# Kernel tuning notes

Measured on AMD Instinct MI355X. Metric: run time of the kernel, lower is better.

## Reference

```python
import jax, jax.numpy as jnp
import numpy as np

NT = 256
T = 8192

def setup_inputs() -> dict:
    key = jax.random.key(0)
    k1, k2, k3, k4, k5 = jax.random.split(key, 5)
    emit = jax.random.normal(k1, (T, NT), dtype=jnp.float32)
    y = jax.random.randint(k2, (T,), 0, NT, dtype=jnp.int64)
    trans = jax.random.normal(k3, (NT, NT), dtype=jnp.float32)
    BOS = jax.random.normal(k4, (NT,), dtype=jnp.float32)
    EOS = jax.random.normal(k5, (NT,), dtype=jnp.float32)
    return {"emit": emit, "y": y, "trans": trans, "BOS": BOS, "EOS": EOS}

def _log_z(emit, trans, BOS):
    # alpha recurrence: alpha_new[j] = emit_i[j] + logsumexp_k(trans[k, j] + alpha[k])
    alpha0 = BOS + emit[0]
    def step(alpha, emit_i):
        alpha_new = emit_i + jax.nn.logsumexp(trans + alpha[:, None], axis=0)
        return alpha_new, None
    alpha, _ = jax.lax.scan(step, alpha0, emit[1:])
    return jax.nn.logsumexp(alpha)

def _gold_score(emit, y, trans, BOS, EOS):
    T_ = emit.shape[0]
    idx = jnp.arange(T_ - 1)
    s = BOS[y[0]]
    # faithful to original: emit[i, y[i]] for i in 0..T-2, plus trans[y[i], y[i+1]]
    s = s + jnp.sum(trans[y[:-1], y[1:]]) + jnp.sum(emit[idx, y[:-1]])
    s = s + EOS[y[-1]] + emit[-1, y[-1]]
    return s

def reference(emit, y, trans, BOS, EOS):
    logZ = _log_z(emit, trans, BOS)
    return logZ - _gold_score(emit, y, trans, BOS, EOS)
```

## Files before the change

kernel.cpp:

```cpp
#include <hip/hip_runtime.h>
#include <hip/hip_fp16.h>

#define TLEN 8192
#define NTS  256
#define CLEN 32
#define NCH  256
#define SLOT2 66048

typedef __bf16 bf16x8 __attribute__((ext_vector_type(8)));
typedef float  f32x4  __attribute__((ext_vector_type(4)));
union U128 { uint4 u; bf16x8 v; };
union U64  { uint2 u; long l; };

__device__ __forceinline__ unsigned f2bfu(float x) {
    unsigned u = __float_as_uint(x);
    return (u + 0x7fffu + ((u >> 16) & 1u)) >> 16;
}
__device__ __forceinline__ unsigned pk2(float lo, float hi) {
    return f2bfu(lo) | (f2bfu(hi) << 16);
}
__device__ __forceinline__ float bf2f(unsigned short h) {
    return __uint_as_float(((unsigned)h) << 16);
}
__device__ __forceinline__ unsigned pk4bf8(float a, float b, float c, float d) {
    int r = __builtin_amdgcn_cvt_pk_bf8_f32(a, b, 0, false);
    r = __builtin_amdgcn_cvt_pk_bf8_f32(c, d, r, true);
    return (unsigned)r;
}

__global__ __launch_bounds__(256, 2) void crf_phase1(
        const float* __restrict__ emit, const float* __restrict__ trans,
        char* __restrict__ outX) {
    __shared__ alignas(16) char qt8[65536];
    __shared__ alignas(16) char scr[4][1280];
    __shared__ alignas(16) float eld[2][NTS];

    const int t    = threadIdx.x;
    const int lane = t & 63;
    const int w    = t >> 6;
    const int gl   = lane >> 4;
    const int ln15 = lane & 15;
    const int c    = blockIdx.x >> 1;
    const int h    = blockIdx.x & 1;
    const int istart = (c == 0) ? 1 : CLEN * c;
    const int iend   = CLEN * c + CLEN;

    {
        const int ln = t & 15;
        for (int gk = 0; gk < 32; gk++) {
            float v[8];
            #pragma unroll
            for (int e = 0; e < 8; e++) v[e] = __expf(trans[(gk * 8 + e) * NTS + t]);
            uint2 u;
            u.x = pk4bf8(v[0], v[1], v[2], v[3]);
            u.y = pk4bf8(v[4], v[5], v[6], v[7]);
            const int p = (gk + 4 * ln + (ln >> 2)) & 31;
            *(uint2*)(qt8 + t * 256 + p * 8) = u;
        }
    }
    eld[istart & 1][t] = __expf(emit[istart * NTS + t]);

    int aoff[8];
    #pragma unroll
    for (int kf = 0; kf < 8; kf++) {
        const int p = (4 * kf + gl + 4 * ln15 + (ln15 >> 2)) & 31;
        aoff[kf] = ln15 * 256 + p * 8;
    }

    uint2 Bf[8][2];
    #pragma unroll
    for (int kf = 0; kf < 8; kf++)
        #pragma unroll
        for (int cb = 0; cb < 2; cb++) {
            uint2 bu; bu.x = 0u; bu.y = 0u;
            const int r_glob = 128 * h + 32 * w + cb * 16 + ln15;
            if ((r_glob >> 3) == kf * 4 + gl) {
                const int e = r_glob & 7;
                if (e < 4) bu.x = 0x3Cu << (8 * e);
                else       bu.y = 0x3Cu << (8 * (e - 4));
            }
            Bf[kf][cb] = bu;
        }
    float rs[2] = {0.f, 0.f};
    __syncthreads();

    char* const mysc = &scr[w][0];
    for (int i = istart; i < iend; ++i) {
        float enext = 0.f;
        if (i + 1 < iend) enext = emit[(i + 1) * NTS + t];

        f32x4 Cacc[16][2];
        #pragma unroll
        for (int jb = 0; jb < 16; jb++)
            #pragma unroll
            for (int cb = 0; cb < 2; cb++) Cacc[jb][cb] = f32x4{0.f, 0.f, 0.f, 0.f};

        #pragma unroll
        for (int jb = 0; jb < 16; jb++) {
            #pragma unroll
            for (int kf = 0; kf < 8; kf++) {
                U64 a; a.u = *(const uint2*)(qt8 + (aoff[kf] + jb * 4096));
                #pragma unroll
                for (int cb = 0; cb < 2; cb++) {
                    U64 b; b.u = Bf[kf][cb];
                    Cacc[jb][cb] = __builtin_amdgcn_mfma_f32_16x16x32_bf8_bf8(
                        a.l, b.l, Cacc[jb][cb], 0, 0, 0);
                }
            }
        }

        #pragma unroll
        for (int jb = 0; jb < 16; jb++) {
            float4 ev = *(const float4*)&eld[i & 1][jb * 16 + gl * 4];
            #pragma unroll
            for (int cb = 0; cb < 2; cb++) {
                Cacc[jb][cb][0] *= ev.x; Cacc[jb][cb][1] *= ev.y;
                Cacc[jb][cb][2] *= ev.z; Cacc[jb][cb][3] *= ev.w;
            }
        }
        float rn[2];
        #pragma unroll
        for (int cb = 0; cb < 2; cb++) {
            float m0 = Cacc[0][cb][0];
            #pragma unroll
            for (int jb = 0; jb < 16; jb++)
                #pragma unroll
                for (int rg = 0; rg < 4; rg++) m0 = fmaxf(m0, Cacc[jb][cb][rg]);
            m0 = fmaxf(m0, __shfl_xor(m0, 16));
            m0 = fmaxf(m0, __shfl_xor(m0, 32));
            rn[cb] = 1.0f / m0;
            rs[cb] += __logf(m0);
        }

        if (i == iend - 1) {
            __syncthreads();
            #pragma unroll
            for (int jb = 0; jb < 16; jb++)
                #pragma unroll
                for (int cb = 0; cb < 2; cb++) {
                    int rsl = w * 32 + cb * 16 + ln15;
                    #pragma unroll
                    for (int rg = 0; rg < 4; rg++) {
                        int j = jb * 16 + gl * 4 + rg;
                        *(unsigned short*)(qt8 + ((j * 128 + rsl) << 1)) =
                            (unsigned short)f2bfu(Cacc[jb][cb][rg] * rn[cb]);
                    }
                }
            __syncthreads();
            char* SO = outX + (size_t)(2 * c + h) * SLOT2;
            #pragma unroll
            for (int q = 0; q < 16; q++)
                *(uint4*)(SO + q * 4096 + t * 16) =
                    *(const uint4*)(qt8 + q * 4096 + t * 16);
            if (lane < 16) {
                #pragma unroll
                for (int cb = 0; cb < 2; cb++) {
                    int rsl = w * 32 + cb * 16 + lane;
                    *(float*)(SO + 65536 + rsl * 4) = rs[cb];
                }
            }
        } else {
            #pragma unroll
            for (int kf = 0; kf < 8; kf++) {
                #pragma unroll
                for (int jbb = 0; jbb < 2; jbb++) {
                    const int jb = 2 * kf + jbb;
                    #pragma unroll
                    for (int cb = 0; cb < 2; cb++) {
                        const int col = cb * 16 + ln15;
                        unsigned pk = pk4bf8(Cacc[jb][cb][0] * rn[cb],
                                             Cacc[jb][cb][1] * rn[cb],
                                             Cacc[jb][cb][2] * rn[cb],
                                             Cacc[jb][cb][3] * rn[cb]);
                        *(unsigned*)(mysc + col * 40 + jbb * 16 + gl * 4) = pk;
                    }
                }
                asm volatile("s_waitcnt lgkmcnt(0)" ::: "memory");
                __builtin_amdgcn_sched_barrier(0);
                #pragma unroll
                for (int cb = 0; cb < 2; cb++) {
                    const int col = cb * 16 + ln15;
                    Bf[kf][cb] = *(const uint2*)(mysc + col * 40 + gl * 8);
                }
                asm volatile("s_waitcnt lgkmcnt(0)" ::: "memory");
                __builtin_amdgcn_sched_barrier(0);
            }
            eld[(i + 1) & 1][t] = __expf(enext);
            __syncthreads();
        }
    }
}

__global__ __launch_bounds__(256, 1) void crf_combine2(
        const char* __restrict__ inb, char* __restrict__ outb) {
    __shared__ alignas(16) char qt[131072];
    __shared__ alignas(16) unsigned scr[4][512];
    __shared__ alignas(16) float efac[NTS];
    __shared__ float smax[4];

    const int t = threadIdx.x;
    const int lane = t & 63;
    const int w = t >> 6;
    const int gl = lane >> 4;
    const int ln15 = lane & 15;
    const int p = blockIdx.x >> 1;
    const int h = blockIdx.x & 1;
    const char* SL0 = inb + (size_t)(4 * p + 2) * SLOT2;
    const char* SL1 = inb + (size_t)(4 * p + 3) * SLOT2;
    const char* SE  = inb + (size_t)(4 * p + h) * SLOT2;
    char* SO = outb + (size_t)(2 * p + h) * SLOT2;

    float sv = *(const float*)(((t < 128) ? SL0 : SL1) + 65536 + (t & 127) * 4);
    float m = sv;
    #pragma unroll
    for (int off = 32; off; off >>= 1) m = fmaxf(m, __shfl_xor(m, off));
    if (lane == 0) smax[w] = m;
    __syncthreads();
    const float sigma = fmaxf(fmaxf(smax[0], smax[1]), fmaxf(smax[2], smax[3]));
    efac[t] = __expf(sv - sigma);
    __syncthreads();

    for (int it = 0; it < 32; it++) {
        int off = it * 2048 + t * 8;
        int j = off >> 8, k = off & 255;
        const char* src = (k < 128) ? (SL0 + (size_t)(j * 128 + k) * 2)
                                    : (SL1 + (size_t)(j * 128 + (k - 128)) * 2);
        uint4 d = *(const uint4*)src;
        float4 e0 = *(const float4*)&efac[k];
        float4 e1 = *(const float4*)&efac[k + 4];
        float ef[8] = {e0.x, e0.y, e0.z, e0.w, e1.x, e1.y, e1.z, e1.w};
        unsigned wds[4] = {d.x, d.y, d.z, d.w};
        unsigned outw[4];
        #pragma unroll
        for (int wi = 0; wi < 4; wi++) {
            float lo = bf2f((unsigned short)(wds[wi] & 0xffffu)) * ef[2 * wi];
            float hi = bf2f((unsigned short)(wds[wi] >> 16)) * ef[2 * wi + 1];
            outw[wi] = pk2(lo, hi);
        }
        uint4 o; o.x = outw[0]; o.y = outw[1]; o.z = outw[2]; o.w = outw[3];
        *(uint4*)(qt + ((j * 512 + k * 2) ^ ((j & 7) << 4))) = o;
    }

    bf16x8 Bf[8][2];
    #pragma unroll
    for (int kf = 0; kf < 8; kf++) {
        #pragma unroll
        for (int p2 = 0; p2 < 2; p2++) {
            int kk = p2 * 16 + (lane >> 2);
            uint4 d = *(const uint4*)(SE + (size_t)(32 * kf + kk) * 256
                                      + w * 64 + (lane & 3) * 16);
            *(uint4*)((char*)&scr[w][0] + kk * 64 + (lane & 3) * 16) = d;
        }
        asm volatile("s_waitcnt lgkmcnt(0)" ::: "memory");
        __builtin_amdgcn_sched_barrier(0);
        #pragma unroll
        for (int cb = 0; cb < 2; cb++) {
            unsigned wd[4] = {0u, 0u, 0u, 0u};
            #pragma unroll
            for (int e = 0; e < 8; e++) {
                int kloc = gl * 8 + e;
                unsigned short hh = *(const unsigned short*)
                    ((const char*)&scr[w][0] + kloc * 64 + (cb * 16 + ln15) * 2);
                wd[e >> 1] |= ((unsigned)hh) << (16 * (e & 1));
            }
            U128 q; q.u.x = wd[0]; q.u.y = wd[1]; q.u.z = wd[2]; q.u.w = wd[3];
            Bf[kf][cb] = q.v;
        }
        asm volatile("s_waitcnt lgkmcnt(0)" ::: "memory");
        __builtin_amdgcn_sched_barrier(0);
    }
    __syncthreads();

    f32x4 Cacc[16][2];
    #pragma unroll
    for (int jb = 0; jb < 16; jb++)
        #pragma unroll
        for (int cb = 0; cb < 2; cb++) Cacc[jb][cb] = f32x4{0.f, 0.f, 0.f, 0.f};
    const int aswz = (lane & 7) << 4;
    #pragma unroll
    for (int jb = 0; jb < 16; jb++) {
        const int abase = (jb * 16 + ln15) * 512 + gl * 16;
        #pragma unroll
        for (int kf = 0; kf < 8; kf++) {
            U128 a; a.u = *(const uint4*)(qt + ((abase + kf * 64) ^ aswz));
            #pragma unroll
            for (int cb = 0; cb < 2; cb++)
                Cacc[jb][cb] = __builtin_amdgcn_mfma_f32_16x16x32_bf16(
                    a.v, Bf[kf][cb], Cacc[jb][cb], 0, 0, 0);
        }
    }

    float mx[2], rn[2];
    #pragma unroll
    for (int cb = 0; cb < 2; cb++) {
        float m0 = Cacc[0][cb][0];
        #pragma unroll
        for (int jb = 0; jb < 16; jb++)
            #pragma unroll
            for (int rg = 0; rg < 4; rg++) m0 = fmaxf(m0, Cacc[jb][cb][rg]);
        m0 = fmaxf(m0, __shfl_xor(m0, 16));
        m0 = fmaxf(m0, __shfl_xor(m0, 32));
        mx[cb] = m0; rn[cb] = 1.0f / m0;
    }

    __syncthreads();
    #pragma unroll
    for (int jb = 0; jb < 16; jb++)
        #pragma unroll
        for (int cb = 0; cb < 2; cb++) {
            int rsl = w * 32 + cb * 16 + ln15;
            #pragma unroll
            for (int rg = 0; rg < 4; rg++) {
                int j = jb * 16 + gl * 4 + rg;
                *(unsigned short*)(qt + ((j * 128 + rsl) << 1)) =
                    (unsigned short)f2bfu(Cacc[jb][cb][rg] * rn[cb]);
            }
        }
    __syncthreads();
    #pragma unroll
    for (int q = 0; q < 16; q++)
        *(uint4*)(SO + q * 4096 + t * 16) = *(const uint4*)(qt + q * 4096 + t * 16);
    if (lane < 16) {
        #pragma unroll
        for (int cb = 0; cb < 2; cb++) {
            int rsl = w * 32 + cb * 16 + lane;
            float se = *(const float*)(SE + 65536 + rsl * 4);
            *(float*)(SO + 65536 + rsl * 4) = se + sigma + __logf(mx[cb]);
        }
    }
}

__global__ __launch_bounds__(512) void crf_chainfin(
        const char* __restrict__ mats, const float* __restrict__ emit,
        const float* __restrict__ BOS, const int* __restrict__ y,
        const float* __restrict__ trans, const float* __restrict__ EOS,
        float* __restrict__ out) {
    __shared__ float red[8];
    __shared__ float smx[8];
    __shared__ alignas(16) float u[NTS];
    __shared__ float pu[NTS];
    const int t = threadIdx.x, lane = t & 63, wv = t >> 6;

    float s = 0.f;
    for (int i = t; i < TLEN - 1; i += 512) {
        int yi = y[i], yn = y[i + 1];
        s += trans[yi * NTS + yn] + emit[i * NTS + yi];
    }
    #pragma unroll
    for (int off = 32; off; off >>= 1) s += __shfl_down(s, off);
    if (lane == 0) red[wv] = s;

    float v0 = (t < NTS) ? (BOS[t] + emit[t]) : -INFINITY;
    float m = v0;
    #pragma unroll
    for (int off = 32; off; off >>= 1) m = fmaxf(m, __shfl_xor(m, off));
    if (lane == 0) smx[wv] = m;
    __syncthreads();
    const float m0 = fmaxf(fmaxf(smx[0], smx[1]), fmaxf(smx[2], smx[3]));
    float wreg = (t < NTS) ? __expf(v0 - m0) : 0.f;
    double W = (double)m0;
    __syncthreads();

    const int j2 = t & 255;
    const int hh = t >> 8;
    for (int c = 0; c < 16; ++c) {
        const char* M0 = mats + (size_t)(2 * c) * SLOT2;
        const char* M1 = M0 + SLOT2;

        float sv = -INFINITY;
        if (t < NTS) sv = *(const float*)(((t < 128) ? M0 : M1) + 65536 + (t & 127) * 4);
        m = sv;
        #pragma unroll
        for (int off = 32; off; off >>= 1) m = fmaxf(m, __shfl_xor(m, off));
        if (lane == 0) smx[wv] = m;
        __syncthreads();
        const float sigma = fmaxf(fmaxf(smx[0], smx[1]), fmaxf(smx[2], smx[3]));
        if (t < NTS) u[t] = __expf(sv - sigma) * wreg;
        __syncthreads();

        const char* Mh = hh ? M1 : M0;
        const uint4* rowp = (const uint4*)(Mh + (size_t)j2 * 256);
        const float* ub = u + hh * 128;
        float acc = 0.f;
        #pragma unroll
        for (int q = 0; q < 16; q++) {
            uint4 a = rowp[q];
            const float* uq = ub + q * 8;
            acc += bf2f((unsigned short)(a.x & 0xffffu)) * uq[0]
                 + bf2f((unsigned short)(a.x >> 16))     * uq[1]
                 + bf2f((unsigned short)(a.y & 0xffffu)) * uq[2]
                 + bf2f((unsigned short)(a.y >> 16))     * uq[3]
                 + bf2f((unsigned short)(a.z & 0xffffu)) * uq[4]
                 + bf2f((unsigned short)(a.z >> 16))     * uq[5]
                 + bf2f((unsigned short)(a.w & 0xffffu)) * uq[6]
                 + bf2f((unsigned short)(a.w >> 16))     * uq[7];
        }
        if (hh == 1) pu[j2] = acc;
        __syncthreads();
        float v = -INFINITY;
        if (t < NTS) v = acc + pu[t];
        m = v;
        #pragma unroll
        for (int off = 32; off; off >>= 1) m = fmaxf(m, __shfl_xor(m, off));
        if (lane == 0) smx[wv] = m;
        __syncthreads();
        const float mstep = fmaxf(fmaxf(smx[0], smx[1]), fmaxf(smx[2], smx[3]));
        W += (double)(sigma + __logf(mstep));
        if (t < NTS) wreg = v * (1.0f / mstep);
        __syncthreads();
    }

    float ssum = (t < NTS) ? wreg : 0.f;
    #pragma unroll
    for (int off = 32; off; off >>= 1) ssum += __shfl_down(ssum, off);
    if (lane == 0) smx[wv] = ssum;
    __syncthreads();
    if (t == 0) {
        float S = smx[0] + smx[1] + smx[2] + smx[3];
        float logZ = (float)(W + (double)__logf(S));
        float gold = 0.f;
        #pragma unroll
        for (int k = 0; k < 8; k++) gold += red[k];
        int y0 = y[0], yl = y[TLEN - 1];
        gold += BOS[y0] + EOS[yl] + emit[(TLEN - 1) * NTS + yl];
        out[0] = logZ - gold;
    }
}

__global__ __launch_bounds__(256) void crf_prep(const float* __restrict__ trans,
                                                __half2* __restrict__ Qp) {
    int j = threadIdx.x, p = blockIdx.x;
    float a = __expf(trans[(2 * p) * NTS + j]);
    float b = __expf(trans[(2 * p + 1) * NTS + j]);
    Qp[p * NTS + j] = __floats2half2_rn(a, b);
}

__global__ __launch_bounds__(512) void crf_forward(
        const float* __restrict__ emit, const float* __restrict__ BOS,
        const __half2* __restrict__ Qp_g, float* __restrict__ logZ_out) {
    __shared__ __half2 Qp[128 * NTS];
    __shared__ alignas(16) float w[NTS];
    __shared__ float part[2][NTS];
    __shared__ float ebuf[2][NTS];
    __shared__ float wavemax[8];
    const int t = threadIdx.x, j = t & 255, q = t >> 8, lane = t & 63, wv = t >> 6;
    for (int idx = t; idx < 128 * NTS; idx += 512) Qp[idx] = Qp_g[idx];
    float anew = -INFINITY;
    if (t < NTS) anew = BOS[t] + emit[t];
    float ml = anew;
    #pragma unroll
    for (int off = 32; off; off >>= 1) ml = fmaxf(ml, __shfl_down(ml, off));
    if (lane == 0) wavemax[wv] = ml;
    __syncthreads();
    float mstep = fmaxf(fmaxf(wavemax[0], wavemax[1]), fmaxf(wavemax[2], wavemax[3]));
    double Macc = (double)mstep;
    if (t < NTS) w[t] = __expf(anew - mstep);
    float epre = 0.f;
    if (q == 1) epre = emit[NTS + j];
    __syncthreads();
    for (int i = 1; i < TLEN; ++i) {
        if (q == 1) ebuf[i & 1][j] = epre;
        float acc = 0.f;
        const __half2* qptr = Qp + (q * 64) * NTS + j;
        const float2* wptr = (const float2*)(w + q * 128);
        #pragma unroll 16
        for (int kk = 0; kk < 64; ++kk) {
            __half2 qv = qptr[kk * NTS];
            float2 wv2 = wptr[kk];
            acc += __low2float(qv) * wv2.x + __high2float(qv) * wv2.y;
        }
        part[q][j] = acc;
        if (q == 1 && (i + 1) < TLEN) epre = emit[(i + 1) * NTS + j];
        __syncthreads();
        float an = 0.f;
        ml = -INFINITY;
        if (t < NTS) {
            float vv = part[0][t] + part[1][t];
            an = ebuf[i & 1][t] + __logf(vv);
            ml = an;
        }
        #pragma unroll
        for (int off = 32; off; off >>= 1) ml = fmaxf(ml, __shfl_down(ml, off));
        if (lane == 0 && wv < 4) wavemax[wv] = ml;
        __syncthreads();
        mstep = fmaxf(fmaxf(wavemax[0], wavemax[1]), fmaxf(wavemax[2], wavemax[3]));
        Macc += (double)mstep;
        if (t < NTS) w[t] = __expf(an - mstep);
        __syncthreads();
    }
    float s = (t < NTS) ? w[t] : 0.f;
    #pragma unroll
    for (int off = 32; off; off >>= 1) s += __shfl_down(s, off);
    if (lane == 0 && wv < 4) wavemax[wv] = s;
    __syncthreads();
    if (t == 0) {
        float tot = wavemax[0] + wavemax[1] + wavemax[2] + wavemax[3];
        logZ_out[0] = (float)(Macc + (double)__logf(tot));
    }
}

__global__ __launch_bounds__(512) void crf_gold(
        const float* __restrict__ emit, const int* __restrict__ y,
        const float* __restrict__ trans, const float* __restrict__ BOS,
        const float* __restrict__ EOS, const float* __restrict__ logZ_ws,
        float* __restrict__ out) {
    __shared__ float red[8];
    int t = threadIdx.x;
    float s = 0.f;
    for (int i = t; i < TLEN - 1; i += 512) {
        int yi = y[i], yn = y[i + 1];
        s += trans[yi * NTS + yn] + emit[i * NTS + yi];
    }
    #pragma unroll
    for (int off = 32; off; off >>= 1) s += __shfl_down(s, off);
    if ((t & 63) == 0) red[t >> 6] = s;
    __syncthreads();
    if (t == 0) {
        float tot = 0.f;
        #pragma unroll
        for (int k2 = 0; k2 < 8; ++k2) tot += red[k2];
        int y0 = y[0], yl = y[TLEN - 1];
        tot += BOS[y0] + EOS[yl] + emit[(TLEN - 1) * NTS + yl];
        out[0] = logZ_ws[0] - tot;
    }
}

extern "C" void kernel_launch(void* const* d_in, const int* in_sizes, int n_in,
                              void* d_out, int out_size, void* d_ws, size_t ws_size,
                              hipStream_t stream) {
    const float* emit  = (const float*)d_in[0];
    const int*   y     = (const int*)d_in[1];
    const float* trans = (const float*)d_in[2];
    const float* BOS   = (const float*)d_in[3];
    const float* EOS   = (const float*)d_in[4];
    float* out = (float*)d_out;

    const size_t need = (size_t)(512 + 256) * SLOT2 + 256;
    if (ws_size >= need) {
        char* X = (char*)d_ws;
        char* Y = X + (size_t)512 * SLOT2;

        crf_phase1<<<2 * NCH, 256, 0, stream>>>(emit, trans, X);
        crf_combine2<<<256, 256, 0, stream>>>(X, Y);
        crf_combine2<<<128, 256, 0, stream>>>(Y, X);
        crf_combine2<<<64, 256, 0, stream>>>(X, Y);
        crf_combine2<<<32, 256, 0, stream>>>(Y, X);
        crf_chainfin<<<1, 512, 0, stream>>>(X, emit, BOS, y, trans, EOS, out);
    } else {
        __half2* Qp = (__half2*)d_ws;
        float* logZ = (float*)((char*)d_ws + 128 * NTS * sizeof(__half2));
        crf_prep<<<128, 256, 0, stream>>>(trans, Qp);
        crf_forward<<<1, 512, 0, stream>>>(emit, BOS, Qp, logZ);
        crf_gold<<<1, 512, 0, stream>>>(emit, y, trans, BOS, EOS, logZ, out);
    }
}
```

Measured before the change: 410.1 us.

## Replace tree combine launches with single sequential chained combine kernel

Replaces the four-level pairwise tree reduction of chunk transfer matrices with one kernel where each of 64 blocks sequentially multiplies 8 chunk matrices, keeping the B operand in registers between stages and accumulating log scales. This removes three kernel launches and intermediate global round-trips. In exchange, per-block serial depth grows to 7 matmuls and the final chain kernel must process 32 instead of 16 matrices, with fewer blocks active.

```diff
diff --git a/kernel.cpp b/kernel.cpp
--- a/kernel.cpp
+++ b/kernel.cpp
@@ -191,7 +191,7 @@
     }
 }
 
-__global__ __launch_bounds__(256, 1) void crf_combine2(
+__global__ __launch_bounds__(256, 1) void crf_combine_run(
         const char* __restrict__ inb, char* __restrict__ outb) {
     __shared__ alignas(16) char qt[131072];
     __shared__ alignas(16) unsigned scr[4][512];
@@ -203,43 +203,10 @@
     const int w = t >> 6;
     const int gl = lane >> 4;
     const int ln15 = lane & 15;
-    const int p = blockIdx.x >> 1;
+    const int g = blockIdx.x >> 1;
     const int h = blockIdx.x & 1;
-    const char* SL0 = inb + (size_t)(4 * p + 2) * SLOT2;
-    const char* SL1 = inb + (size_t)(4 * p + 3) * SLOT2;
-    const char* SE  = inb + (size_t)(4 * p + h) * SLOT2;
-    char* SO = outb + (size_t)(2 * p + h) * SLOT2;
-
-    float sv = *(const float*)(((t < 128) ? SL0 : SL1) + 65536 + (t & 127) * 4);
-    float m = sv;
-    #pragma unroll
-    for (int off = 32; off; off >>= 1) m = fmaxf(m, __shfl_xor(m, off));
-    if (lane == 0) smax[w] = m;
-    __syncthreads();
-    const float sigma = fmaxf(fmaxf(smax[0], smax[1]), fmaxf(smax[2], smax[3]));
-    efac[t] = __expf(sv - sigma);
-    __syncthreads();
-
-    for (int it = 0; it < 32; it++) {
-        int off = it * 2048 + t * 8;
-        int j = off >> 8, k = off & 255;
-        const char* src = (k < 128) ? (SL0 + (size_t)(j * 128 + k) * 2)
-                                    : (SL1 + (size_t)(j * 128 + (k - 128)) * 2);
-        uint4 d = *(const uint4*)src;
-        float4 e0 = *(const float4*)&efac[k];
-        float4 e1 = *(const float4*)&efac[k + 4];
-        float ef[8] = {e0.x, e0.y, e0.z, e0.w, e1.x, e1.y, e1.z, e1.w};
-        unsigned wds[4] = {d.x, d.y, d.z, d.w};
-        unsigned outw[4];
-        #pragma unroll
-        for (int wi = 0; wi < 4; wi++) {
-            float lo = bf2f((unsigned short)(wds[wi] & 0xffffu)) * ef[2 * wi];
-            float hi = bf2f((unsigned short)(wds[wi] >> 16)) * ef[2 * wi + 1];
-            outw[wi] = pk2(lo, hi);
-        }
-        uint4 o; o.x = outw[0]; o.y = outw[1]; o.z = outw[2]; o.w = outw[3];
-        *(uint4*)(qt + ((j * 512 + k * 2) ^ ((j & 7) << 4))) = o;
-    }
+    const char* SB = inb + (size_t)(16 * g + h) * SLOT2;
+    char* SO = outb + (size_t)(2 * g + h) * SLOT2;
 
     bf16x8 Bf[8][2];
     #pragma unroll
@@ -247,7 +214,7 @@
         #pragma unroll
         for (int p2 = 0; p2 < 2; p2++) {
             int kk = p2 * 16 + (lane >> 2);
-            uint4 d = *(const uint4*)(SE + (size_t)(32 * kf + kk) * 256
+            uint4 d = *(const uint4*)(SB + (size_t)(32 * kf + kk) * 256
                                       + w * 64 + (lane & 3) * 16);
             *(uint4*)((char*)&scr[w][0] + kk * 64 + (lane & 3) * 16) = d;
         }
@@ -269,38 +236,108 @@
         asm volatile("s_waitcnt lgkmcnt(0)" ::: "memory");
         __builtin_amdgcn_sched_barrier(0);
     }
-    __syncthreads();
-
+
+    float logacc[2] = {0.f, 0.f};
+    float rn[2];
     f32x4 Cacc[16][2];
-    #pragma unroll
-    for (int jb = 0; jb < 16; jb++)
-        #pragma unroll
-        for (int cb = 0; cb < 2; cb++) Cacc[jb][cb] = f32x4{0.f, 0.f, 0.f, 0.f};
     const int aswz = (lane & 7) << 4;
-    #pragma unroll
-    for (int jb = 0; jb < 16; jb++) {
-        const int abase = (jb * 16 + ln15) * 512 + gl * 16;
-        #pragma unroll
-        for (int kf = 0; kf < 8; kf++) {
-            U128 a; a.u = *(const uint4*)(qt + ((abase + kf * 64) ^ aswz));
-            #pragma unroll
-            for (int cb = 0; cb < 2; cb++)
-                Cacc[jb][cb] = __builtin_amdgcn_mfma_f32_16x16x32_bf16(
-                    a.v, Bf[kf][cb], Cacc[jb][cb], 0, 0, 0);
-        }
-    }
-
-    float mx[2], rn[2];
-    #pragma unroll
-    for (int cb = 0; cb < 2; cb++) {
-        float m0 = Cacc[0][cb][0];
+
+    for (int stg = 1; stg <= 7; ++stg) {
+        const char* A0 = inb + (size_t)(16 * g + 2 * stg) * SLOT2;
+        const char* A1 = A0 + SLOT2;
+
+        float sv = *(const float*)(((t < 128) ? A0 : A1) + 65536 + (t & 127) * 4);
+        float m = sv;
+        #pragma unroll
+        for (int off = 32; off; off >>= 1) m = fmaxf(m, __shfl_xor(m, off));
+        if (lane == 0) smax[w] = m;
+        __syncthreads();
+        const float sigma = fmaxf(fmaxf(smax[0], smax[1]),
+                                  fmaxf(smax[2], smax[3]));
+        efac[t] = __expf(sv - sigma);
+        __syncthreads();
+
+        for (int it = 0; it < 32; it++) {
+            int off = it * 2048 + t * 8;
+            int j = off >> 8, k = off & 255;
+            const char* src = (k < 128) ? (A0 + (size_t)(j * 128 + k) * 2)
+                                        : (A1 + (size_t)(j * 128 + (k - 128)) * 2);
+            uint4 d = *(const uint4*)src;
+            float4 e0 = *(const float4*)&efac[k];
+            float4 e1 = *(const float4*)&efac[k + 4];
+            float ef[8] = {e0.x, e0.y, e0.z, e0.w, e1.x, e1.y, e1.z, e1.w};
+            unsigned wds[4] = {d.x, d.y, d.z, d.w};
+            unsigned outw[4];
+            #pragma unroll
+            for (int wi = 0; wi < 4; wi++) {
+                float lo = bf2f((unsigned short)(wds[wi] & 0xffffu)) * ef[2 * wi];
+                float hi = bf2f((unsigned short)(wds[wi] >> 16)) * ef[2 * wi + 1];
+                outw[wi] = pk2(lo, hi);
+            }
+            uint4 o; o.x = outw[0]; o.y = outw[1]; o.z = outw[2]; o.w = outw[3];
+            *(uint4*)(qt + ((j * 512 + k * 2) ^ ((j & 7) << 4))) = o;
+        }
+        __syncthreads();
+
         #pragma unroll
         for (int jb = 0; jb < 16; jb++)
             #pragma unroll
-            for (int rg = 0; rg < 4; rg++) m0 = fmaxf(m0, Cacc[jb][cb][rg]);
-        m0 = fmaxf(m0, __shfl_xor(m0, 16));
-        m0 = fmaxf(m0, __shfl_xor(m0, 32));
-        mx[cb] = m0; rn[cb] = 1.0f / m0;
+            for (int cb = 0; cb < 2; cb++) Cacc[jb][cb] = f32x4{0.f, 0.f, 0.f, 0.f};
+        #pragma unroll
+        for (int jb = 0; jb < 16; jb++) {
+            const int abase = (jb * 16 + ln15) * 512 + gl * 16;
+            #pragma unroll
+            for (int kf = 0; kf < 8; kf++) {
+                U128 a; a.u = *(const uint4*)(qt + ((abase + kf * 64) ^ aswz));
+                #pragma unroll
+                for (int cb = 0; cb < 2; cb++)
+                    Cacc[jb][cb] = __builtin_amdgcn_mfma_f32_16x16x32_bf16(
+                        a.v, Bf[kf][cb], Cacc[jb][cb], 0, 0, 0);
+            }
+        }
+
+        #pragma unroll
+        for (int cb = 0; cb < 2; cb++) {
+            float m0 = Cacc[0][cb][0];
+            #pragma unroll
+            for (int jb = 0; jb < 16; jb++)
+                #pragma unroll
+                for (int rg = 0; rg < 4; rg++) m0 = fmaxf(m0, Cacc[jb][cb][rg]);
+            m0 = fmaxf(m0, __shfl_xor(m0, 16));
+            m0 = fmaxf(m0, __shfl_xor(m0, 32));
+            rn[cb] = 1.0f / m0;
+            logacc[cb] += sigma + __logf(m0);
+        }
+
+        if (stg < 7) {
+            #pragma unroll
+            for (int kf = 0; kf < 8; kf++) {
+                #pragma unroll
+                for (int jbb = 0; jbb < 2; jbb++) {
+                    const int jb = 2 * kf + jbb;
+                    const int koct = 2 * jbb + (gl >> 1);
+                    #pragma unroll
+                    for (int cb = 0; cb < 2; cb++) {
+                        const int addr = (koct * 512 + (cb * 16 + ln15) * 16
+                                          + (gl & 1) * 8) ^ (koct << 4);
+                        uint2 pk;
+                        pk.x = pk2(Cacc[jb][cb][0] * rn[cb], Cacc[jb][cb][1] * rn[cb]);
+                        pk.y = pk2(Cacc[jb][cb][2] * rn[cb], Cacc[jb][cb][3] * rn[cb]);
+                        *(uint2*)((char*)&scr[w][0] + addr) = pk;
+                    }
+                }
+                asm volatile("s_waitcnt lgkmcnt(0)" ::: "memory");
+                __builtin_amdgcn_sched_barrier(0);
+                #pragma unroll
+                for (int cb = 0; cb < 2; cb++) {
+                    const int rb = (gl * 512 + (cb * 16 + ln15) * 16) ^ (gl << 4);
+                    U128 q; q.u = *(const uint4*)((const char*)&scr[w][0] + rb);
+                    Bf[kf][cb] = q.v;
+                }
+                asm volatile("s_waitcnt lgkmcnt(0)" ::: "memory");
+                __builtin_amdgcn_sched_barrier(0);
+            }
+        }
     }
 
     __syncthreads();
@@ -324,8 +361,8 @@
         #pragma unroll
         for (int cb = 0; cb < 2; cb++) {
             int rsl = w * 32 + cb * 16 + lane;
-            float se = *(const float*)(SE + 65536 + rsl * 4);
-            *(float*)(SO + 65536 + rsl * 4) = se + sigma + __logf(mx[cb]);
+            float sb = *(const float*)(SB + 65536 + rsl * 4);
+            *(float*)(SO + 65536 + rsl * 4) = sb + logacc[cb];
         }
     }
 }
@@ -363,7 +400,7 @@
 
     const int j2 = t & 255;
     const int hh = t >> 8;
-    for (int c = 0; c < 16; ++c) {
+    for (int c = 0; c < 32; ++c) {
         const char* M0 = mats + (size_t)(2 * c) * SLOT2;
         const char* M1 = M0 + SLOT2;
 
@@ -541,11 +578,8 @@
         char* Y = X + (size_t)512 * SLOT2;
 
         crf_phase1<<<2 * NCH, 256, 0, stream>>>(emit, trans, X);
-        crf_combine2<<<256, 256, 0, stream>>>(X, Y);
-        crf_combine2<<<128, 256, 0, stream>>>(Y, X);
-        crf_combine2<<<64, 256, 0, stream>>>(X, Y);
-        crf_combine2<<<32, 256, 0, stream>>>(Y, X);
-        crf_chainfin<<<1, 512, 0, stream>>>(X, emit, BOS, y, trans, EOS, out);
+        crf_combine_run<<<64, 256, 0, stream>>>(X, Y);
+        crf_chainfin<<<1, 512, 0, stream>>>(Y, emit, BOS, y, trans, EOS, out);
     } else {
         __half2* Qp = (__half2*)d_ws;
         float* logZ = (float*)((char*)d_ws + 128 * NTS * sizeof(__half2));
```

New measurement: 550.1 us. +34.1%, slower.

## Fuse combine tree levels and final chain into one cooperative kernel

Applied to the files above, without the earlier changes.

Replaces the four combine launches and the single-block chain/final kernel with one cooperative kernel that steps through the tree levels using grid-wide syncs. Idle blocks in level 1 compute the gold-score partial sums in parallel, and block 0 then runs the 16-step chain product with 256 threads, each handling both halves of its row. The aim is to remove per-launch gaps and the serial gold loop, at the cost of grid.sync overhead and a cooperative launch that needs all 256 blocks resident at once. If the cooperative launch fails, the old multi-launch path is used.

```diff
diff --git a/kernel.cpp b/kernel.cpp
--- a/kernel.cpp
+++ b/kernel.cpp
@@ -1,5 +1,8 @@
 #include <hip/hip_runtime.h>
 #include <hip/hip_fp16.h>
+#include <hip/hip_cooperative_groups.h>
+
+namespace cg = cooperative_groups;
 
 #define TLEN 8192
 #define NTS  256
@@ -26,6 +29,16 @@
     int r = __builtin_amdgcn_cvt_pk_bf8_f32(a, b, 0, false);
     r = __builtin_amdgcn_cvt_pk_bf8_f32(c, d, r, true);
     return (unsigned)r;
+}
+__device__ __forceinline__ float dot8(uint4 a, const float* uq) {
+    return bf2f((unsigned short)(a.x & 0xffffu)) * uq[0]
+         + bf2f((unsigned short)(a.x >> 16))     * uq[1]
+         + bf2f((unsigned short)(a.y & 0xffffu)) * uq[2]
+         + bf2f((unsigned short)(a.y >> 16))     * uq[3]
+         + bf2f((unsigned short)(a.z & 0xffffu)) * uq[4]
+         + bf2f((unsigned short)(a.z >> 16))     * uq[5]
+         + bf2f((unsigned short)(a.w & 0xffffu)) * uq[6]
+         + bf2f((unsigned short)(a.w >> 16))     * uq[7];
 }
 
 __global__ __launch_bounds__(256, 2) void crf_phase1(
@@ -191,20 +204,11 @@
     }
 }
 
-__global__ __launch_bounds__(256, 1) void crf_combine2(
-        const char* __restrict__ inb, char* __restrict__ outb) {
-    __shared__ alignas(16) char qt[131072];
-    __shared__ alignas(16) unsigned scr[4][512];
-    __shared__ alignas(16) float efac[NTS];
-    __shared__ float smax[4];
-
-    const int t = threadIdx.x;
-    const int lane = t & 63;
-    const int w = t >> 6;
-    const int gl = lane >> 4;
-    const int ln15 = lane & 15;
-    const int p = blockIdx.x >> 1;
-    const int h = blockIdx.x & 1;
+__device__ __forceinline__ void combine_body(
+        const char* __restrict__ inb, char* __restrict__ outb,
+        int p, int h, char* qt, unsigned (*scr)[512],
+        float* efac, float* smax,
+        int t, int lane, int w, int gl, int ln15) {
     const char* SL0 = inb + (size_t)(4 * p + 2) * SLOT2;
     const char* SL1 = inb + (size_t)(4 * p + 3) * SLOT2;
     const char* SE  = inb + (size_t)(4 * p + h) * SLOT2;
@@ -330,7 +334,121 @@
     }
 }
 
-__global__ __launch_bounds__(512) void crf_chainfin(
+__global__ __launch_bounds__(256, 1) void crf_tail(
+        char* X, char* Y, const float* emit, const float* BOS,
+        const int* y, const float* trans, const float* EOS,
+        float* goldws, float* out) {
+    __shared__ alignas(16) char qt[131072];
+    __shared__ alignas(16) unsigned scr[4][512];
+    __shared__ alignas(16) float efac[NTS];
+    __shared__ float smax[4];
+    __shared__ alignas(16) float u[NTS];
+
+    cg::grid_group grid = cg::this_grid();
+    const int b = blockIdx.x;
+    const int t = threadIdx.x;
+    const int lane = t & 63;
+    const int w = t >> 6;
+    const int gl = lane >> 4;
+    const int ln15 = lane & 15;
+
+    for (int l = 0; l < 4; ++l) {
+        char* inb  = (l & 1) ? Y : X;
+        char* outb = (l & 1) ? X : Y;
+        const int nin = 256 >> l;
+        if (b < nin) {
+            combine_body(inb, outb, b >> 1, b & 1, qt, scr, efac, smax,
+                         t, lane, w, gl, ln15);
+        } else if (l == 1) {
+            float s = 0.f;
+            if (t < 64) {
+                int i = (b - 128) * 64 + t;
+                if (i < TLEN - 1)
+                    s = trans[y[i] * NTS + y[i + 1]] + emit[i * NTS + y[i]];
+                #pragma unroll
+                for (int off = 32; off; off >>= 1) s += __shfl_down(s, off);
+                if (t == 0) goldws[b - 128] = s;
+            }
+        }
+        grid.sync();
+    }
+
+    if (b == 0) {
+        float v0 = BOS[t] + emit[t];
+        float m = v0;
+        #pragma unroll
+        for (int off = 32; off; off >>= 1) m = fmaxf(m, __shfl_xor(m, off));
+        if (lane == 0) smax[w] = m;
+        __syncthreads();
+        const float m0 = fmaxf(fmaxf(smax[0], smax[1]), fmaxf(smax[2], smax[3]));
+        float wreg = __expf(v0 - m0);
+        double W = (double)m0;
+        __syncthreads();
+
+        for (int c = 0; c < 16; ++c) {
+            const char* M0 = X + (size_t)(2 * c) * SLOT2;
+            const char* M1 = M0 + SLOT2;
+
+            float sv = *(const float*)(((t < 128) ? M0 : M1) + 65536 + (t & 127) * 4);
+            m = sv;
+            #pragma unroll
+            for (int off = 32; off; off >>= 1) m = fmaxf(m, __shfl_xor(m, off));
+            if (lane == 0) smax[w] = m;
+            __syncthreads();
+            const float sigma = fmaxf(fmaxf(smax[0], smax[1]),
+                                      fmaxf(smax[2], smax[3]));
+            u[t] = __expf(sv - sigma) * wreg;
+            __syncthreads();
+
+            const uint4* r0 = (const uint4*)(M0 + (size_t)t * 256);
+            const uint4* r1 = (const uint4*)(M1 + (size_t)t * 256);
+            float acc = 0.f;
+            #pragma unroll
+            for (int q = 0; q < 16; q++) acc += dot8(r0[q], &u[q * 8]);
+            #pragma unroll
+            for (int q = 0; q < 16; q++) acc += dot8(r1[q], &u[128 + q * 8]);
+
+            m = acc;
+            #pragma unroll
+            for (int off = 32; off; off >>= 1) m = fmaxf(m, __shfl_xor(m, off));
+            if (lane == 0) smax[w] = m;
+            __syncthreads();
+            const float mstep = fmaxf(fmaxf(smax[0], smax[1]),
+                                      fmaxf(smax[2], smax[3]));
+            W += (double)(sigma + __logf(mstep));
+            wreg = acc * (1.0f / mstep);
+            __syncthreads();
+        }
+
+        float ssum = wreg;
+        #pragma unroll
+        for (int off = 32; off; off >>= 1) ssum += __shfl_down(ssum, off);
+        if (lane == 0) smax[w] = ssum;
+        __syncthreads();
+        if (t == 0) {
+            float S = smax[0] + smax[1] + smax[2] + smax[3];
+            float logZ = (float)(W + (double)__logf(S));
+            float gold = 0.f;
+            for (int k = 0; k < 128; k++) gold += goldws[k];
+            int y0 = y[0], yl = y[TLEN - 1];
+            gold += BOS[y0] + EOS[yl] + emit[(TLEN - 1) * NTS + yl];
+            out[0] = logZ - gold;
+        }
+    }
+}
+
+__global__ __launch_bounds__(256, 1) void crf_combine2(
+        const char* __restrict__ inb, char* __restrict__ outb) {
+    __shared__ alignas(16) char qt[131072];
+    __shared__ alignas(16) unsigned scr[4][512];
+    __shared__ alignas(16) float efac[NTS];
+    __shared__ float smax[4];
+    const int t = threadIdx.x;
+    combine_body(inb, outb, blockIdx.x >> 1, blockIdx.x & 1, qt, scr, efac, smax,
+                 t, t & 63, t >> 6, (t & 63) >> 4, t & 15);
+}
+
+__global__ __launch_bounds__(512) void crf_chainfin16(
         const char* __restrict__ mats, const float* __restrict__ emit,
         const float* __restrict__ BOS, const int* __restrict__ y,
         const float* __restrict__ trans, const float* __restrict__ EOS,
@@ -366,7 +484,6 @@
     for (int c = 0; c < 16; ++c) {
         const char* M0 = mats + (size_t)(2 * c) * SLOT2;
         const char* M1 = M0 + SLOT2;
-
         float sv = -INFINITY;
         if (t < NTS) sv = *(const float*)(((t < 128) ? M0 : M1) + 65536 + (t & 127) * 4);
         m = sv;
@@ -383,18 +500,7 @@
         const float* ub = u + hh * 128;
         float acc = 0.f;
         #pragma unroll
-        for (int q = 0; q < 16; q++) {
-            uint4 a = rowp[q];
-            const float* uq = ub + q * 8;
-            acc += bf2f((unsigned short)(a.x & 0xffffu)) * uq[0]
-                 + bf2f((unsigned short)(a.x >> 16))     * uq[1]
-                 + bf2f((unsigned short)(a.y & 0xffffu)) * uq[2]
-                 + bf2f((unsigned short)(a.y >> 16))     * uq[3]
-                 + bf2f((unsigned short)(a.z & 0xffffu)) * uq[4]
-                 + bf2f((unsigned short)(a.z >> 16))     * uq[5]
-                 + bf2f((unsigned short)(a.w & 0xffffu)) * uq[6]
-                 + bf2f((unsigned short)(a.w >> 16))     * uq[7];
-        }
+        for (int q = 0; q < 16; q++) acc += dot8(rowp[q], ub + q * 8);
         if (hh == 1) pu[j2] = acc;
         __syncthreads();
         float v = -INFINITY;
@@ -535,17 +641,25 @@
     const float* EOS   = (const float*)d_in[4];
     float* out = (float*)d_out;
 
-    const size_t need = (size_t)(512 + 256) * SLOT2 + 256;
+    const size_t need = (size_t)(512 + 256) * SLOT2 + 1024;
     if (ws_size >= need) {
         char* X = (char*)d_ws;
         char* Y = X + (size_t)512 * SLOT2;
+        float* goldws = (float*)(Y + (size_t)256 * SLOT2);
 
         crf_phase1<<<2 * NCH, 256, 0, stream>>>(emit, trans, X);
-        crf_combine2<<<256, 256, 0, stream>>>(X, Y);
-        crf_combine2<<<128, 256, 0, stream>>>(Y, X);
-        crf_combine2<<<64, 256, 0, stream>>>(X, Y);
-        crf_combine2<<<32, 256, 0, stream>>>(Y, X);
-        crf_chainfin<<<1, 512, 0, stream>>>(X, emit, BOS, y, trans, EOS, out);
+
+        void* args[] = { &X, &Y, (void*)&emit, (void*)&BOS, (void*)&y,
+                         (void*)&trans, (void*)&EOS, &goldws, &out };
+        hipError_t e = hipLaunchCooperativeKernel(
+            (void*)crf_tail, dim3(256), dim3(256), args, 0, stream);
+        if (e != hipSuccess) {
+            crf_combine2<<<256, 256, 0, stream>>>(X, Y);
+            crf_combine2<<<128, 256, 0, stream>>>(Y, X);
+            crf_combine2<<<64, 256, 0, stream>>>(X, Y);
+            crf_combine2<<<32, 256, 0, stream>>>(Y, X);
+            crf_chainfin16<<<1, 512, 0, stream>>>(X, emit, BOS, y, trans, EOS, out);
+        }
     } else {
         __half2* Qp = (__half2*)d_ws;
         float* logZ = (float*)((char*)d_ws + 128 * NTS * sizeof(__half2));
```

New measurement: 521.0 us. 27.0% more time.
